# Kernel tuning notes

Measured on AMD Instinct MI355X. Metric: run time of the kernel, lower is better.

Reference implementation:

```python
import jax, jax.numpy as jnp
import numpy as np

N = 50000
E = 800000
IN_C = 128
HID = 64
HEADS = 2
OUT_C = 40
NEG_SLOPE = 0.2


def glorot(key, shape):
    fan_in, fan_out = shape[0], shape[-1]
    lim = jnp.sqrt(6.0 / (fan_in + fan_out))
    return jax.random.uniform(key, shape, jnp.float32, -lim, lim)


def setup_inputs() -> dict:
    key = jax.random.key(0)
    ks = jax.random.split(key, 10)
    x = jax.random.normal(ks[0], (N, IN_C), jnp.float32)
    edge_index = jax.random.randint(ks[1], (2, E), 0, N, jnp.int32)
    # layer 1: heads=2, concat -> out features HEADS*HID
    W1 = glorot(ks[2], (IN_C, HEADS * HID))
    att_src1 = glorot(ks[3], (HEADS, HID))
    att_dst1 = glorot(ks[4], (HEADS, HID))
    b1 = jnp.zeros((HEADS * HID,), jnp.float32)
    # layer 2: out_heads=1, concat=False (mean over the single head)
    W2 = glorot(ks[5], (HEADS * HID, 1 * OUT_C))
    att_src2 = glorot(ks[6], (1, OUT_C))
    att_dst2 = glorot(ks[7], (1, OUT_C))
    b2 = jnp.zeros((OUT_C,), jnp.float32)
    return {"x": x, "edge_index": edge_index,
            "W1": W1, "att_src1": att_src1, "att_dst1": att_dst1, "b1": b1,
            "W2": W2, "att_src2": att_src2, "att_dst2": att_dst2, "b2": b2}


def _segment_softmax(logits, seg, num_segments):
    # logits: [E, H]; softmax over edges sharing the same destination node
    m = jax.ops.segment_max(logits, seg, num_segments=num_segments)
    m = jnp.where(jnp.isfinite(m), m, 0.0)
    e = jnp.exp(logits - m[seg])
    s = jax.ops.segment_sum(e, seg, num_segments=num_segments)
    return e / (s[seg] + 1e-16)


def _gat_conv(x, src, dst, W, a_src, a_dst, b, concat, n_nodes):
    H, C = a_src.shape
    h = (x @ W).reshape(n_nodes, H, C)                    # [N, H, C]
    al_src = jnp.einsum('nhc,hc->nh', h, a_src)           # [N, H]
    al_dst = jnp.einsum('nhc,hc->nh', h, a_dst)           # [N, H]
    e = jax.nn.leaky_relu(al_src[src] + al_dst[dst], NEG_SLOPE)  # [E, H]
    alpha = _segment_softmax(e, dst, n_nodes)             # [E, H]
    msg = h[src] * alpha[:, :, None]                      # [E, H, C]
    out = jax.ops.segment_sum(msg, dst, num_segments=n_nodes)
    out = out.reshape(n_nodes, H * C) if concat else out.mean(axis=1)
    return out + b


def reference(x, edge_index, W1, att_src1, att_dst1, b1, W2, att_src2, att_dst2, b2):
    n_nodes = x.shape[0]
    loop = jnp.arange(n_nodes, dtype=edge_index.dtype)
    src = jnp.concatenate([edge_index[0], loop])  # add self loops
    dst = jnp.concatenate([edge_index[1], loop])
    # eval mode: dropout is identity, use_bn=False -> no batchnorm
    h = _gat_conv(x, src, dst, W1, att_src1, att_dst1, b1, True, n_nodes)
    h = jax.nn.elu(h)
    out = _gat_conv(h, src, dst, W2, att_src2, att_dst2, b2, False, n_nodes)
    return out
```

## Files before the change

kernel.cpp:

```cpp
#include <hip/hip_runtime.h>
#include <hip/hip_fp16.h>

#define NEG_SLOPE 0.2f

typedef _Float16 f16x8 __attribute__((ext_vector_type(8)));
typedef float f32x4 __attribute__((ext_vector_type(4)));

__device__ __forceinline__ int h2i(__half2 h) { return *(int*)&h; }
__device__ __forceinline__ __half2 i2h(int i) { return *(__half2*)&i; }
__device__ __forceinline__ float lrelu(float v) { return (v > 0.f) ? v : NEG_SLOPE * v; }
__device__ __forceinline__ int pkmax(int a, int b) {
    int r;
    asm("v_pk_max_f16 %0, %1, %2" : "=v"(r) : "v"(a), "v"(b));
    return r;
}
__device__ __forceinline__ __half selh(int r, int packed) {
    return (r < 8) ? __low2half(i2h(packed)) : __high2half(i2h(packed));
}

union U16x8 { uint4 u; __half2 h[4]; };
union U16x4 { uint2 u; __half2 h[2]; };

__global__ __launch_bounds__(256) void k_pack(const float* __restrict__ W1,
                                              const float* __restrict__ W2,
                                              _Float16* __restrict__ bp1,
                                              _Float16* __restrict__ bp2,
                                              int* __restrict__ cnt, int N) {
    int idx = blockIdx.x * 256 + threadIdx.x;
    if (idx < N) cnt[idx] = 0;
    if (idx < 16384) {
        int j = idx & 7, l = (idx >> 3) & 63, nt = (idx >> 9) & 7, ks = idx >> 12;
        int k = ks * 32 + (l >> 4) * 8 + j;
        int col = nt * 16 + (l & 15);
        bp1[idx] = (_Float16)W1[k * 128 + col];
    }
    int idx2 = idx - 16384;
    if (idx2 >= 0 && idx2 < 6144) {
        int j = idx2 & 7, l = (idx2 >> 3) & 63, q = idx2 >> 9;
        int nt = q % 3, ks = q / 3;
        int k = ks * 32 + (l >> 4) * 8 + j;
        int col = nt * 16 + (l & 15);
        bp2[idx2] = (col < 40) ? (_Float16)W2[k * 40 + col] : (_Float16)0.f;
    }
}

__global__ void k_bucket(const int* __restrict__ ei, int* __restrict__ cnt,
                         int* __restrict__ colell, int E, int ps) {
    int p = blockIdx.x & 7;
    int e = (blockIdx.x >> 3) * blockDim.x + threadIdx.x;
    if (e >= E) return;
    int d = ei[E + e];
    int lo = p * ps;
    if (d < lo || d >= lo + ps) return;
    int s = ei[e];
    int rank = atomicAdd(&cnt[d], 1);
    if (rank < 64) colell[(size_t)d * 64 + rank] = s;
}

__global__ __launch_bounds__(256) void k_gemm1(
    const float* __restrict__ x, const _Float16* __restrict__ bp1,
    const float* __restrict__ as1, const float* __restrict__ ad1,
    __half2* __restrict__ h1h, float* __restrict__ alsrc, float* __restrict__ aldst,
    int N) {
    int w = threadIdx.x >> 6, l = threadIdx.x & 63;
    int n0 = blockIdx.x * 64 + w * 16;
    int li = l & 15, lg = l >> 4;
    int arow = n0 + li;
    f16x8 a[4];
#pragma unroll
    for (int ks = 0; ks < 4; ks++) {
        float4 p0 = make_float4(0, 0, 0, 0), p1 = make_float4(0, 0, 0, 0);
        if (arow < N) {
            const float4* src = (const float4*)(x + (size_t)arow * 128 + ks * 32 + lg * 8);
            p0 = src[0];
            p1 = src[1];
        }
        f16x8 t;
        t[0] = (_Float16)p0.x; t[1] = (_Float16)p0.y; t[2] = (_Float16)p0.z; t[3] = (_Float16)p0.w;
        t[4] = (_Float16)p1.x; t[5] = (_Float16)p1.y; t[6] = (_Float16)p1.z; t[7] = (_Float16)p1.w;
        a[ks] = t;
    }
    f32x4 acc[8];
#pragma unroll
    for (int nt = 0; nt < 8; nt++) acc[nt] = (f32x4){0.f, 0.f, 0.f, 0.f};
    const f16x8* bp = (const f16x8*)bp1;
#pragma unroll
    for (int nt = 0; nt < 8; nt++)
#pragma unroll
        for (int ks = 0; ks < 4; ks++)
            acc[nt] = __builtin_amdgcn_mfma_f32_16x16x32_f16(a[ks], bp[(ks * 8 + nt) * 64 + l],
                                                             acc[nt], 0, 0, 0);
    float as1v[8], ad1v[8];
#pragma unroll
    for (int nt = 0; nt < 8; nt++) {
        as1v[nt] = as1[nt * 16 + li];
        ad1v[nt] = ad1[nt * 16 + li];
    }
#pragma unroll
    for (int r = 0; r < 4; r++) {
        float ps0 = 0, ps1 = 0, pd0 = 0, pd1 = 0;
#pragma unroll
        for (int nt = 0; nt < 4; nt++) {
            ps0 = fmaf(acc[nt][r], as1v[nt], ps0);
            pd0 = fmaf(acc[nt][r], ad1v[nt], pd0);
        }
#pragma unroll
        for (int nt = 4; nt < 8; nt++) {
            ps1 = fmaf(acc[nt][r], as1v[nt], ps1);
            pd1 = fmaf(acc[nt][r], ad1v[nt], pd1);
        }
#pragma unroll
        for (int o = 1; o < 16; o <<= 1) {
            ps0 += __shfl_xor(ps0, o);
            ps1 += __shfl_xor(ps1, o);
            pd0 += __shfl_xor(pd0, o);
            pd1 += __shfl_xor(pd1, o);
        }
        int node = n0 + lg * 4 + r;
        if (li == 0 && node < N) {
            alsrc[node * 2] = ps0;
            alsrc[node * 2 + 1] = ps1;
            aldst[node * 2] = pd0;
            aldst[node * 2 + 1] = pd1;
        }
    }
#pragma unroll
    for (int nt = 0; nt < 8; nt++)
#pragma unroll
        for (int r = 0; r < 4; r++) {
            float v = acc[nt][r];
            float p = __shfl_down(v, 1);
            int node = n0 + lg * 4 + r;
            if ((l & 1) == 0 && node < N)
                h1h[(size_t)node * 64 + nt * 8 + (li >> 1)] = __floats2half2_rn(v, p);
        }
}

__global__ __launch_bounds__(256) void k_gemm2(
    const _Float16* __restrict__ hf, const _Float16* __restrict__ bp2,
    const float* __restrict__ as2, const float* __restrict__ ad2,
    __half2* __restrict__ h2h, float* __restrict__ alsrc, float* __restrict__ aldst,
    int N) {
    int w = threadIdx.x >> 6, l = threadIdx.x & 63;
    int n0 = blockIdx.x * 64 + w * 16;
    int li = l & 15, lg = l >> 4;
    int arow = n0 + li;
    const f16x8* hfv = (const f16x8*)hf;
    f16x8 a[4];
#pragma unroll
    for (int ks = 0; ks < 4; ks++) {
        f16x8 t;
        if (arow < N) {
            t = hfv[(size_t)arow * 16 + ks * 4 + lg];
        } else {
#pragma unroll
            for (int k = 0; k < 8; k++) t[k] = (_Float16)0.f;
        }
        a[ks] = t;
    }
    f32x4 acc[3];
#pragma unroll
    for (int nt = 0; nt < 3; nt++) acc[nt] = (f32x4){0.f, 0.f, 0.f, 0.f};
    const f16x8* bp = (const f16x8*)bp2;
#pragma unroll
    for (int nt = 0; nt < 3; nt++)
#pragma unroll
        for (int ks = 0; ks < 4; ks++)
            acc[nt] = __builtin_amdgcn_mfma_f32_16x16x32_f16(a[ks], bp[(ks * 3 + nt) * 64 + l],
                                                             acc[nt], 0, 0, 0);
    float as2v[3], ad2v[3];
#pragma unroll
    for (int nt = 0; nt < 3; nt++) {
        int col = nt * 16 + li;
        as2v[nt] = (col < 40) ? as2[col] : 0.f;
        ad2v[nt] = (col < 40) ? ad2[col] : 0.f;
    }
#pragma unroll
    for (int r = 0; r < 4; r++) {
        float ps = 0, pd = 0;
#pragma unroll
        for (int nt = 0; nt < 3; nt++) {
            ps = fmaf(acc[nt][r], as2v[nt], ps);
            pd = fmaf(acc[nt][r], ad2v[nt], pd);
        }
#pragma unroll
        for (int o = 1; o < 16; o <<= 1) {
            ps += __shfl_xor(ps, o);
            pd += __shfl_xor(pd, o);
        }
        int node = n0 + lg * 4 + r;
        if (li == 0 && node < N) {
            alsrc[node] = ps;
            aldst[node] = pd;
        }
    }
#pragma unroll
    for (int nt = 0; nt < 3; nt++)
#pragma unroll
        for (int r = 0; r < 4; r++) {
            float v = acc[nt][r];
            float p = __shfl_down(v, 1);
            int node = n0 + lg * 4 + r;
            int col = nt * 16 + li;
            if ((l & 1) == 0 && col < 40 && node < N)
                h2h[(size_t)node * 20 + nt * 8 + (li >> 1)] = __floats2half2_rn(v, p);
        }
}

__global__ __launch_bounds__(256) void k_gather1(
    const int* __restrict__ cnt, const int* __restrict__ colell,
    const _Float16* __restrict__ h1, const float2* __restrict__ alsrc,
    const float2* __restrict__ aldst, const float4* __restrict__ b1v,
    _Float16* __restrict__ hf, int N) {
    int wid = (int)(((size_t)blockIdx.x * blockDim.x + threadIdx.x) >> 6);
    int lane = threadIdx.x & 63;
    if (wid >= N) return;
    int g = lane >> 4, r = lane & 15;
    float2 asn = alsrc[wid], ad = aldst[wid];
    float ls0 = lrelu(asn.x + ad.x);
    float ls1 = lrelu(asn.y + ad.y);
    int nb = min(cnt[wid], 64);
    int sv = 0;
    float l0 = -1e30f, l1 = -1e30f;
    if (lane < nb) {
        sv = colell[(size_t)wid * 64 + lane];
        float2 av = alsrc[sv];
        l0 = lrelu(av.x + ad.x);
        l1 = lrelu(av.y + ad.y);
    }
    int lpi = h2i(__floats2half2_rn(l0, l1));
#pragma unroll
    for (int o = 32; o > 0; o >>= 1) lpi = pkmax(lpi, __shfl_xor(lpi, o));
    __half2 lp = i2h(lpi);
    float m0 = fmaxf(__low2float(lp), ls0);
    float m1 = fmaxf(__high2float(lp), ls1);
    float e0 = (lane < nb) ? __expf(l0 - m0) : 0.f;
    float e1 = (lane < nb) ? __expf(l1 - m1) : 0.f;
    int we = h2i(__floats2half2_rn(e0, e1));
    float lsh = (r < 8) ? ls0 : ls1;
    float mh = (r < 8) ? m0 : m1;
    __half esh = __float2half((g == 0) ? __expf(lsh - mh) : 0.f);
    float s_part = __half2float(esh);
    __half2 esp = __half2half2(esh);
    U16x8 hs;
    hs.u = *(const uint4*)(h1 + (size_t)wid * 128 + r * 8);
    __half2 a0 = __hmul2(hs.h[0], esp), a1 = __hmul2(hs.h[1], esp),
            a2 = __hmul2(hs.h[2], esp), a3 = __hmul2(hs.h[3], esp);
    if (nb > 0) {
        int i0 = __shfl(sv, g),      p0 = __shfl(we, g);
        int i1 = __shfl(sv, 4 + g),  p1 = __shfl(we, 4 + g);
        int i2 = __shfl(sv, 8 + g),  p2 = __shfl(we, 8 + g);
        int i3 = __shfl(sv, 12 + g), p3 = __shfl(we, 12 + g);
        U16x8 hA, hB, hC, hD;
        hA.u = *(const uint4*)(h1 + (size_t)i0 * 128 + r * 8);
        hB.u = *(const uint4*)(h1 + (size_t)i1 * 128 + r * 8);
        hC.u = *(const uint4*)(h1 + (size_t)i2 * 128 + r * 8);
        hD.u = *(const uint4*)(h1 + (size_t)i3 * 128 + r * 8);
        __half wA = selh(r, p0), wB = selh(r, p1), wC = selh(r, p2), wD = selh(r, p3);
        for (int j = 16; j < nb; j += 4) {
            int i4 = __shfl(sv, j + g), p4 = __shfl(we, j + g);
            U16x8 hN;
            hN.u = *(const uint4*)(h1 + (size_t)i4 * 128 + r * 8);
            __half2 ww = __half2half2(wA);
            s_part += __half2float(wA);
            a0 = __hfma2(ww, hA.h[0], a0);
            a1 = __hfma2(ww, hA.h[1], a1);
            a2 = __hfma2(ww, hA.h[2], a2);
            a3 = __hfma2(ww, hA.h[3], a3);
            hA = hB; wA = wB;
            hB = hC; wB = wC;
            hC = hD; wC = wD;
            hD = hN; wD = selh(r, p4);
        }
        {
            __half2 ww = __half2half2(wA);
            s_part += __half2float(wA);
            a0 = __hfma2(ww, hA.h[0], a0); a1 = __hfma2(ww, hA.h[1], a1);
            a2 = __hfma2(ww, hA.h[2], a2); a3 = __hfma2(ww, hA.h[3], a3);
        }
        {
            __half2 ww = __half2half2(wB);
            s_part += __half2float(wB);
            a0 = __hfma2(ww, hB.h[0], a0); a1 = __hfma2(ww, hB.h[1], a1);
            a2 = __hfma2(ww, hB.h[2], a2); a3 = __hfma2(ww, hB.h[3], a3);
        }
        {
            __half2 ww = __half2half2(wC);
            s_part += __half2float(wC);
            a0 = __hfma2(ww, hC.h[0], a0); a1 = __hfma2(ww, hC.h[1], a1);
            a2 = __hfma2(ww, hC.h[2], a2); a3 = __hfma2(ww, hC.h[3], a3);
        }
        {
            __half2 ww = __half2half2(wD);
            s_part += __half2float(wD);
            a0 = __hfma2(ww, hD.h[0], a0); a1 = __hfma2(ww, hD.h[1], a1);
            a2 = __hfma2(ww, hD.h[2], a2); a3 = __hfma2(ww, hD.h[3], a3);
        }
    }
#pragma unroll
    for (int o = 16; o < 64; o <<= 1) {
        s_part += __shfl_xor(s_part, o);
        a0 = __hadd2(a0, i2h(__shfl_xor(h2i(a0), o)));
        a1 = __hadd2(a1, i2h(__shfl_xor(h2i(a1), o)));
        a2 = __hadd2(a2, i2h(__shfl_xor(h2i(a2), o)));
        a3 = __hadd2(a3, i2h(__shfl_xor(h2i(a3), o)));
    }
    if (g == 0) {
        float inv = 1.f / (s_part + 1e-16f);
        float4 bA = b1v[2 * r], bB = b1v[2 * r + 1];
        float v[8] = {__low2float(a0), __high2float(a0), __low2float(a1), __high2float(a1),
                      __low2float(a2), __high2float(a2), __low2float(a3), __high2float(a3)};
        float vb[8] = {bA.x, bA.y, bA.z, bA.w, bB.x, bB.y, bB.z, bB.w};
        U16x8 o;
#pragma unroll
        for (int k = 0; k < 8; k += 2) {
            float u0 = fmaf(v[k], inv, vb[k]);
            float u1 = fmaf(v[k + 1], inv, vb[k + 1]);
            u0 = (u0 > 0.f) ? u0 : (__expf(u0) - 1.f);
            u1 = (u1 > 0.f) ? u1 : (__expf(u1) - 1.f);
            o.h[k >> 1] = __floats2half2_rn(u0, u1);
        }
        *(uint4*)(hf + (size_t)wid * 128 + r * 8) = o.u;
    }
}

__global__ __launch_bounds__(256) void k_gather2(
    const int* __restrict__ cnt, const int* __restrict__ colell,
    const _Float16* __restrict__ h2, const float* __restrict__ alsrc,
    const float* __restrict__ aldst, const float4* __restrict__ b2v,
    float4* __restrict__ out4, int N) {
    int wid = (int)(((size_t)blockIdx.x * blockDim.x + threadIdx.x) >> 6);
    int lane = threadIdx.x & 63;
    if (wid >= N) return;
    int g = lane >> 4, r = lane & 15;
    int rc = (r < 10) ? r : 0;
    float ad = aldst[wid];
    float ls = lrelu(alsrc[wid] + ad);
    int nb = min(cnt[wid], 64);
    int sv = 0;
    float l = -1e30f;
    if (lane < nb) {
        sv = colell[(size_t)wid * 64 + lane];
        l = lrelu(alsrc[sv] + ad);
    }
    float m = l;
#pragma unroll
    for (int o = 32; o > 0; o >>= 1) m = fmaxf(m, __shfl_xor(m, o));
    m = fmaxf(m, ls);
    float e = (lane < nb) ? __expf(l - m) : 0.f;
    float es = (g == 0) ? __expf(ls - m) : 0.f;
    float s_part = es;
    __half2 esp = __floats2half2_rn(es, es);
    U16x4 hs;
    hs.u = *(const uint2*)(h2 + (size_t)wid * 40 + rc * 4);
    __half2 a0 = __hmul2(hs.h[0], esp), a1 = __hmul2(hs.h[1], esp);
    if (nb > 0) {
        int i0 = __shfl(sv, g);
        int i1 = __shfl(sv, 4 + g);
        int i2 = __shfl(sv, 8 + g);
        int i3 = __shfl(sv, 12 + g);
        float wA = __shfl(e, g), wB = __shfl(e, 4 + g);
        float wC = __shfl(e, 8 + g), wD = __shfl(e, 12 + g);
        U16x4 hA, hB, hC, hD;
        hA.u = *(const uint2*)(h2 + (size_t)i0 * 40 + rc * 4);
        hB.u = *(const uint2*)(h2 + (size_t)i1 * 40 + rc * 4);
        hC.u = *(const uint2*)(h2 + (size_t)i2 * 40 + rc * 4);
        hD.u = *(const uint2*)(h2 + (size_t)i3 * 40 + rc * 4);
        for (int j = 16; j < nb; j += 4) {
            int i4 = __shfl(sv, j + g);
            float wN = __shfl(e, j + g);
            U16x4 hN;
            hN.u = *(const uint2*)(h2 + (size_t)i4 * 40 + rc * 4);
            __half2 ww = __floats2half2_rn(wA, wA);
            s_part += wA;
            a0 = __hfma2(ww, hA.h[0], a0);
            a1 = __hfma2(ww, hA.h[1], a1);
            hA = hB; wA = wB;
            hB = hC; wB = wC;
            hC = hD; wC = wD;
            hD = hN; wD = wN;
        }
        {
            __half2 ww = __floats2half2_rn(wA, wA);
            s_part += wA;
            a0 = __hfma2(ww, hA.h[0], a0); a1 = __hfma2(ww, hA.h[1], a1);
        }
        {
            __half2 ww = __floats2half2_rn(wB, wB);
            s_part += wB;
            a0 = __hfma2(ww, hB.h[0], a0); a1 = __hfma2(ww, hB.h[1], a1);
        }
        {
            __half2 ww = __floats2half2_rn(wC, wC);
            s_part += wC;
            a0 = __hfma2(ww, hC.h[0], a0); a1 = __hfma2(ww, hC.h[1], a1);
        }
        {
            __half2 ww = __floats2half2_rn(wD, wD);
            s_part += wD;
            a0 = __hfma2(ww, hD.h[0], a0); a1 = __hfma2(ww, hD.h[1], a1);
        }
    }
#pragma unroll
    for (int o = 16; o < 64; o <<= 1) {
        s_part += __shfl_xor(s_part, o);
        a0 = __hadd2(a0, i2h(__shfl_xor(h2i(a0), o)));
        a1 = __hadd2(a1, i2h(__shfl_xor(h2i(a1), o)));
    }
    if (g == 0 && r < 10) {
        float inv = 1.f / (s_part + 1e-16f);
        float4 b = b2v[r];
        float4 o = make_float4(fmaf(__low2float(a0), inv, b.x),
                               fmaf(__high2float(a0), inv, b.y),
                               fmaf(__low2float(a1), inv, b.z),
                               fmaf(__high2float(a1), inv, b.w));
        out4[(size_t)wid * 10 + r] = o;
    }
}

extern "C" void kernel_launch(void* const* d_in, const int* in_sizes, int n_in,
                              void* d_out, int out_size, void* d_ws, size_t ws_size,
                              hipStream_t stream) {
    const float* x   = (const float*)d_in[0];
    const int*   ei  = (const int*)d_in[1];
    const float* W1  = (const float*)d_in[2];
    const float* as1 = (const float*)d_in[3];
    const float* ad1 = (const float*)d_in[4];
    const float* b1  = (const float*)d_in[5];
    const float* W2  = (const float*)d_in[6];
    const float* as2 = (const float*)d_in[7];
    const float* ad2 = (const float*)d_in[8];
    const float* b2  = (const float*)d_in[9];
    int N = in_sizes[0] / 128;
    int E = in_sizes[1] / 2;
    float4* out4 = (float4*)d_out;

    char* ws = (char*)d_ws;
    size_t off = 0;
    auto alloc = [&](size_t bytes) {
        char* p = ws + off;
        off += (bytes + 255) & ~(size_t)255;
        return p;
    };
    int*      cnt    = (int*)alloc((size_t)N * 4);
    int*      colell = (int*)alloc((size_t)N * 64 * 4);
    _Float16* bp1    = (_Float16*)alloc(16384 * 2);
    _Float16* bp2    = (_Float16*)alloc(6144 * 2);
    _Float16* h1h    = (_Float16*)alloc((size_t)N * 128 * 2);
    _Float16* hf     = (_Float16*)alloc((size_t)N * 128 * 2);
    _Float16* h2h    = (_Float16*)alloc((size_t)N * 40 * 2);
    float*    alsrc1 = (float*)alloc((size_t)N * 2 * 4);
    float*    aldst1 = (float*)alloc((size_t)N * 2 * 4);
    float*    alsrc2 = (float*)alloc((size_t)N * 4);
    float*    aldst2 = (float*)alloc((size_t)N * 4);

    dim3 b256(256);
    int ps = (N + 7) / 8;
    int gB = 8 * ((E + 255) / 256);
    int gP = (N > 22528 ? N + 255 : 22528 + 255) / 256;

    k_pack<<<gP, b256, 0, stream>>>(W1, W2, bp1, bp2, cnt, N);
    k_bucket<<<gB, b256, 0, stream>>>(ei, cnt, colell, E, ps);

    int gG = (N + 63) / 64;
    k_gemm1<<<gG, b256, 0, stream>>>(x, bp1, as1, ad1, (__half2*)h1h, alsrc1, aldst1, N);
    k_gather1<<<(int)(((size_t)N * 64 + 255) / 256), b256, 0, stream>>>(
        cnt, colell, h1h, (const float2*)alsrc1, (const float2*)aldst1,
        (const float4*)b1, hf, N);

    k_gemm2<<<gG, b256, 0, stream>>>(hf, bp2, as2, ad2, (__half2*)h2h, alsrc2, aldst2, N);
    k_gather2<<<(int)(((size_t)N * 64 + 255) / 256), b256, 0, stream>>>(
        cnt, colell, h2h, alsrc2, aldst2, (const float4*)b2, out4, N);
}
```

Measured before the change: 126.0 us.

## Fuse layer-2 GEMM into layer-1 gather via shared memory; vectorize edge bucketing

The layer-2 projection (MFMA GEMM plus attention logits) now runs inside the layer-1 gather kernel. Each block's four aggregated node rows are staged in LDS and wave 0 does a 16x16 MFMA tile with only 4 valid rows. This drops the hf intermediate buffer and one kernel launch, saving the global write and reread of the hidden features. The cost is a block-wide barrier, three idle waves during the GEMM, and 12 of 16 MFMA rows wasted. Separately, the bucketing kernel now handles two edges per thread using an int2 load of destinations.

```diff
diff --git a/kernel.cpp b/kernel.cpp
--- a/kernel.cpp
+++ b/kernel.cpp
@@ -47,14 +47,20 @@
 __global__ void k_bucket(const int* __restrict__ ei, int* __restrict__ cnt,
                          int* __restrict__ colell, int E, int ps) {
     int p = blockIdx.x & 7;
-    int e = (blockIdx.x >> 3) * blockDim.x + threadIdx.x;
+    int e = ((blockIdx.x >> 3) * blockDim.x + threadIdx.x) * 2;
     if (e >= E) return;
-    int d = ei[E + e];
-    int lo = p * ps;
-    if (d < lo || d >= lo + ps) return;
-    int s = ei[e];
-    int rank = atomicAdd(&cnt[d], 1);
-    if (rank < 64) colell[(size_t)d * 64 + rank] = s;
+    int lo = p * ps, hi = lo + ps;
+    int2 d2 = *(const int2*)(ei + E + e);
+    if (d2.x >= lo && d2.x < hi) {
+        int s = ei[e];
+        int rank = atomicAdd(&cnt[d2.x], 1);
+        if (rank < 64) colell[(size_t)d2.x * 64 + rank] = s;
+    }
+    if (e + 1 < E && d2.y >= lo && d2.y < hi) {
+        int s = ei[e + 1];
+        int rank = atomicAdd(&cnt[d2.y], 1);
+        if (rank < 64) colell[(size_t)d2.y * 64 + rank] = s;
+    }
 }
 
 __global__ __launch_bounds__(256) void k_gemm1(
@@ -136,191 +142,190 @@
         }
 }
 
-__global__ __launch_bounds__(256) void k_gemm2(
-    const _Float16* __restrict__ hf, const _Float16* __restrict__ bp2,
-    const float* __restrict__ as2, const float* __restrict__ ad2,
-    __half2* __restrict__ h2h, float* __restrict__ alsrc, float* __restrict__ aldst,
-    int N) {
-    int w = threadIdx.x >> 6, l = threadIdx.x & 63;
-    int n0 = blockIdx.x * 64 + w * 16;
-    int li = l & 15, lg = l >> 4;
-    int arow = n0 + li;
-    const f16x8* hfv = (const f16x8*)hf;
-    f16x8 a[4];
-#pragma unroll
-    for (int ks = 0; ks < 4; ks++) {
-        f16x8 t;
-        if (arow < N) {
-            t = hfv[(size_t)arow * 16 + ks * 4 + lg];
-        } else {
-#pragma unroll
-            for (int k = 0; k < 8; k++) t[k] = (_Float16)0.f;
-        }
-        a[ks] = t;
-    }
-    f32x4 acc[3];
-#pragma unroll
-    for (int nt = 0; nt < 3; nt++) acc[nt] = (f32x4){0.f, 0.f, 0.f, 0.f};
-    const f16x8* bp = (const f16x8*)bp2;
-#pragma unroll
-    for (int nt = 0; nt < 3; nt++)
-#pragma unroll
-        for (int ks = 0; ks < 4; ks++)
-            acc[nt] = __builtin_amdgcn_mfma_f32_16x16x32_f16(a[ks], bp[(ks * 3 + nt) * 64 + l],
-                                                             acc[nt], 0, 0, 0);
-    float as2v[3], ad2v[3];
-#pragma unroll
-    for (int nt = 0; nt < 3; nt++) {
-        int col = nt * 16 + li;
-        as2v[nt] = (col < 40) ? as2[col] : 0.f;
-        ad2v[nt] = (col < 40) ? ad2[col] : 0.f;
-    }
-#pragma unroll
-    for (int r = 0; r < 4; r++) {
-        float ps = 0, pd = 0;
-#pragma unroll
-        for (int nt = 0; nt < 3; nt++) {
-            ps = fmaf(acc[nt][r], as2v[nt], ps);
-            pd = fmaf(acc[nt][r], ad2v[nt], pd);
-        }
-#pragma unroll
-        for (int o = 1; o < 16; o <<= 1) {
-            ps += __shfl_xor(ps, o);
-            pd += __shfl_xor(pd, o);
-        }
-        int node = n0 + lg * 4 + r;
-        if (li == 0 && node < N) {
-            alsrc[node] = ps;
-            aldst[node] = pd;
-        }
-    }
-#pragma unroll
-    for (int nt = 0; nt < 3; nt++)
-#pragma unroll
-        for (int r = 0; r < 4; r++) {
-            float v = acc[nt][r];
-            float p = __shfl_down(v, 1);
-            int node = n0 + lg * 4 + r;
-            int col = nt * 16 + li;
-            if ((l & 1) == 0 && col < 40 && node < N)
-                h2h[(size_t)node * 20 + nt * 8 + (li >> 1)] = __floats2half2_rn(v, p);
-        }
-}
-
 __global__ __launch_bounds__(256) void k_gather1(
     const int* __restrict__ cnt, const int* __restrict__ colell,
     const _Float16* __restrict__ h1, const float2* __restrict__ alsrc,
     const float2* __restrict__ aldst, const float4* __restrict__ b1v,
-    _Float16* __restrict__ hf, int N) {
-    int wid = (int)(((size_t)blockIdx.x * blockDim.x + threadIdx.x) >> 6);
+    const _Float16* __restrict__ bp2, const float* __restrict__ as2,
+    const float* __restrict__ ad2, __half2* __restrict__ h2h,
+    float* __restrict__ alsrc2, float* __restrict__ aldst2, int N) {
+    __shared__ __align__(16) _Float16 hfl[4][128];
+    int w = threadIdx.x >> 6;
     int lane = threadIdx.x & 63;
-    if (wid >= N) return;
-    int g = lane >> 4, r = lane & 15;
-    float2 asn = alsrc[wid], ad = aldst[wid];
-    float ls0 = lrelu(asn.x + ad.x);
-    float ls1 = lrelu(asn.y + ad.y);
-    int nb = min(cnt[wid], 64);
-    int sv = 0;
-    float l0 = -1e30f, l1 = -1e30f;
-    if (lane < nb) {
-        sv = colell[(size_t)wid * 64 + lane];
-        float2 av = alsrc[sv];
-        l0 = lrelu(av.x + ad.x);
-        l1 = lrelu(av.y + ad.y);
-    }
-    int lpi = h2i(__floats2half2_rn(l0, l1));
-#pragma unroll
-    for (int o = 32; o > 0; o >>= 1) lpi = pkmax(lpi, __shfl_xor(lpi, o));
-    __half2 lp = i2h(lpi);
-    float m0 = fmaxf(__low2float(lp), ls0);
-    float m1 = fmaxf(__high2float(lp), ls1);
-    float e0 = (lane < nb) ? __expf(l0 - m0) : 0.f;
-    float e1 = (lane < nb) ? __expf(l1 - m1) : 0.f;
-    int we = h2i(__floats2half2_rn(e0, e1));
-    float lsh = (r < 8) ? ls0 : ls1;
-    float mh = (r < 8) ? m0 : m1;
-    __half esh = __float2half((g == 0) ? __expf(lsh - mh) : 0.f);
-    float s_part = __half2float(esh);
-    __half2 esp = __half2half2(esh);
-    U16x8 hs;
-    hs.u = *(const uint4*)(h1 + (size_t)wid * 128 + r * 8);
-    __half2 a0 = __hmul2(hs.h[0], esp), a1 = __hmul2(hs.h[1], esp),
-            a2 = __hmul2(hs.h[2], esp), a3 = __hmul2(hs.h[3], esp);
-    if (nb > 0) {
-        int i0 = __shfl(sv, g),      p0 = __shfl(we, g);
-        int i1 = __shfl(sv, 4 + g),  p1 = __shfl(we, 4 + g);
-        int i2 = __shfl(sv, 8 + g),  p2 = __shfl(we, 8 + g);
-        int i3 = __shfl(sv, 12 + g), p3 = __shfl(we, 12 + g);
-        U16x8 hA, hB, hC, hD;
-        hA.u = *(const uint4*)(h1 + (size_t)i0 * 128 + r * 8);
-        hB.u = *(const uint4*)(h1 + (size_t)i1 * 128 + r * 8);
-        hC.u = *(const uint4*)(h1 + (size_t)i2 * 128 + r * 8);
-        hD.u = *(const uint4*)(h1 + (size_t)i3 * 128 + r * 8);
-        __half wA = selh(r, p0), wB = selh(r, p1), wC = selh(r, p2), wD = selh(r, p3);
-        for (int j = 16; j < nb; j += 4) {
-            int i4 = __shfl(sv, j + g), p4 = __shfl(we, j + g);
-            U16x8 hN;
-            hN.u = *(const uint4*)(h1 + (size_t)i4 * 128 + r * 8);
-            __half2 ww = __half2half2(wA);
-            s_part += __half2float(wA);
-            a0 = __hfma2(ww, hA.h[0], a0);
-            a1 = __hfma2(ww, hA.h[1], a1);
-            a2 = __hfma2(ww, hA.h[2], a2);
-            a3 = __hfma2(ww, hA.h[3], a3);
-            hA = hB; wA = wB;
-            hB = hC; wB = wC;
-            hC = hD; wC = wD;
-            hD = hN; wD = selh(r, p4);
-        }
-        {
-            __half2 ww = __half2half2(wA);
-            s_part += __half2float(wA);
-            a0 = __hfma2(ww, hA.h[0], a0); a1 = __hfma2(ww, hA.h[1], a1);
-            a2 = __hfma2(ww, hA.h[2], a2); a3 = __hfma2(ww, hA.h[3], a3);
-        }
-        {
-            __half2 ww = __half2half2(wB);
-            s_part += __half2float(wB);
-            a0 = __hfma2(ww, hB.h[0], a0); a1 = __hfma2(ww, hB.h[1], a1);
-            a2 = __hfma2(ww, hB.h[2], a2); a3 = __hfma2(ww, hB.h[3], a3);
-        }
-        {
-            __half2 ww = __half2half2(wC);
-            s_part += __half2float(wC);
-            a0 = __hfma2(ww, hC.h[0], a0); a1 = __hfma2(ww, hC.h[1], a1);
-            a2 = __hfma2(ww, hC.h[2], a2); a3 = __hfma2(ww, hC.h[3], a3);
-        }
-        {
-            __half2 ww = __half2half2(wD);
-            s_part += __half2float(wD);
-            a0 = __hfma2(ww, hD.h[0], a0); a1 = __hfma2(ww, hD.h[1], a1);
-            a2 = __hfma2(ww, hD.h[2], a2); a3 = __hfma2(ww, hD.h[3], a3);
-        }
-    }
-#pragma unroll
-    for (int o = 16; o < 64; o <<= 1) {
-        s_part += __shfl_xor(s_part, o);
-        a0 = __hadd2(a0, i2h(__shfl_xor(h2i(a0), o)));
-        a1 = __hadd2(a1, i2h(__shfl_xor(h2i(a1), o)));
-        a2 = __hadd2(a2, i2h(__shfl_xor(h2i(a2), o)));
-        a3 = __hadd2(a3, i2h(__shfl_xor(h2i(a3), o)));
-    }
-    if (g == 0) {
-        float inv = 1.f / (s_part + 1e-16f);
-        float4 bA = b1v[2 * r], bB = b1v[2 * r + 1];
-        float v[8] = {__low2float(a0), __high2float(a0), __low2float(a1), __high2float(a1),
-                      __low2float(a2), __high2float(a2), __low2float(a3), __high2float(a3)};
-        float vb[8] = {bA.x, bA.y, bA.z, bA.w, bB.x, bB.y, bB.z, bB.w};
-        U16x8 o;
-#pragma unroll
-        for (int k = 0; k < 8; k += 2) {
-            float u0 = fmaf(v[k], inv, vb[k]);
-            float u1 = fmaf(v[k + 1], inv, vb[k + 1]);
-            u0 = (u0 > 0.f) ? u0 : (__expf(u0) - 1.f);
-            u1 = (u1 > 0.f) ? u1 : (__expf(u1) - 1.f);
-            o.h[k >> 1] = __floats2half2_rn(u0, u1);
-        }
-        *(uint4*)(hf + (size_t)wid * 128 + r * 8) = o.u;
+    int n0 = blockIdx.x * 4;
+    int wid = n0 + w;
+    if (wid < N) {
+        int g = lane >> 4, r = lane & 15;
+        float2 asn = alsrc[wid], ad = aldst[wid];
+        float ls0 = lrelu(asn.x + ad.x);
+        float ls1 = lrelu(asn.y + ad.y);
+        int nb = min(cnt[wid], 64);
+        int sv = 0;
+        float l0 = -1e30f, l1 = -1e30f;
+        if (lane < nb) {
+            sv = colell[(size_t)wid * 64 + lane];
+            float2 av = alsrc[sv];
+            l0 = lrelu(av.x + ad.x);
+            l1 = lrelu(av.y + ad.y);
+        }
+        int lpi = h2i(__floats2half2_rn(l0, l1));
+#pragma unroll
+        for (int o = 32; o > 0; o >>= 1) lpi = pkmax(lpi, __shfl_xor(lpi, o));
+        __half2 lp = i2h(lpi);
+        float m0 = fmaxf(__low2float(lp), ls0);
+        float m1 = fmaxf(__high2float(lp), ls1);
+        float e0 = (lane < nb) ? __expf(l0 - m0) : 0.f;
+        float e1 = (lane < nb) ? __expf(l1 - m1) : 0.f;
+        int we = h2i(__floats2half2_rn(e0, e1));
+        float lsh = (r < 8) ? ls0 : ls1;
+        float mh = (r < 8) ? m0 : m1;
+        __half esh = __float2half((g == 0) ? __expf(lsh - mh) : 0.f);
+        float s_part = __half2float(esh);
+        __half2 esp = __half2half2(esh);
+        U16x8 hs;
+        hs.u = *(const uint4*)(h1 + (size_t)wid * 128 + r * 8);
+        __half2 a0 = __hmul2(hs.h[0], esp), a1 = __hmul2(hs.h[1], esp),
+                a2 = __hmul2(hs.h[2], esp), a3 = __hmul2(hs.h[3], esp);
+        if (nb > 0) {
+            int i0 = __shfl(sv, g),      p0 = __shfl(we, g);
+            int i1 = __shfl(sv, 4 + g),  p1 = __shfl(we, 4 + g);
+            int i2 = __shfl(sv, 8 + g),  p2 = __shfl(we, 8 + g);
+            int i3 = __shfl(sv, 12 + g), p3 = __shfl(we, 12 + g);
+            U16x8 hA, hB, hC, hD;
+            hA.u = *(const uint4*)(h1 + (size_t)i0 * 128 + r * 8);
+            hB.u = *(const uint4*)(h1 + (size_t)i1 * 128 + r * 8);
+            hC.u = *(const uint4*)(h1 + (size_t)i2 * 128 + r * 8);
+            hD.u = *(const uint4*)(h1 + (size_t)i3 * 128 + r * 8);
+            __half wA = selh(r, p0), wB = selh(r, p1), wC = selh(r, p2), wD = selh(r, p3);
+            for (int j = 16; j < nb; j += 4) {
+                int i4 = __shfl(sv, j + g), p4 = __shfl(we, j + g);
+                U16x8 hN;
+                hN.u = *(const uint4*)(h1 + (size_t)i4 * 128 + r * 8);
+                __half2 ww = __half2half2(wA);
+                s_part += __half2float(wA);
+                a0 = __hfma2(ww, hA.h[0], a0);
+                a1 = __hfma2(ww, hA.h[1], a1);
+                a2 = __hfma2(ww, hA.h[2], a2);
+                a3 = __hfma2(ww, hA.h[3], a3);
+                hA = hB; wA = wB;
+                hB = hC; wB = wC;
+                hC = hD; wC = wD;
+                hD = hN; wD = selh(r, p4);
+            }
+            {
+                __half2 ww = __half2half2(wA);
+                s_part += __half2float(wA);
+                a0 = __hfma2(ww, hA.h[0], a0); a1 = __hfma2(ww, hA.h[1], a1);
+                a2 = __hfma2(ww, hA.h[2], a2); a3 = __hfma2(ww, hA.h[3], a3);
+            }
+            {
+                __half2 ww = __half2half2(wB);
+                s_part += __half2float(wB);
+                a0 = __hfma2(ww, hB.h[0], a0); a1 = __hfma2(ww, hB.h[1], a1);
+                a2 = __hfma2(ww, hB.h[2], a2); a3 = __hfma2(ww, hB.h[3], a3);
+            }
+            {
+                __half2 ww = __half2half2(wC);
+                s_part += __half2float(wC);
+                a0 = __hfma2(ww, hC.h[0], a0); a1 = __hfma2(ww, hC.h[1], a1);
+                a2 = __hfma2(ww, hC.h[2], a2); a3 = __hfma2(ww, hC.h[3], a3);
+            }
+            {
+                __half2 ww = __half2half2(wD);
+                s_part += __half2float(wD);
+                a0 = __hfma2(ww, hD.h[0], a0); a1 = __hfma2(ww, hD.h[1], a1);
+                a2 = __hfma2(ww, hD.h[2], a2); a3 = __hfma2(ww, hD.h[3], a3);
+            }
+        }
+#pragma unroll
+        for (int o = 16; o < 64; o <<= 1) {
+            s_part += __shfl_xor(s_part, o);
+            a0 = __hadd2(a0, i2h(__shfl_xor(h2i(a0), o)));
+            a1 = __hadd2(a1, i2h(__shfl_xor(h2i(a1), o)));
+            a2 = __hadd2(a2, i2h(__shfl_xor(h2i(a2), o)));
+            a3 = __hadd2(a3, i2h(__shfl_xor(h2i(a3), o)));
+        }
+        if (g == 0) {
+            float inv = 1.f / (s_part + 1e-16f);
+            float4 bA = b1v[2 * r], bB = b1v[2 * r + 1];
+            float v[8] = {__low2float(a0), __high2float(a0), __low2float(a1), __high2float(a1),
+                          __low2float(a2), __high2float(a2), __low2float(a3), __high2float(a3)};
+            float vb[8] = {bA.x, bA.y, bA.z, bA.w, bB.x, bB.y, bB.z, bB.w};
+            U16x8 o;
+#pragma unroll
+            for (int k = 0; k < 8; k += 2) {
+                float u0 = fmaf(v[k], inv, vb[k]);
+                float u1 = fmaf(v[k + 1], inv, vb[k + 1]);
+                u0 = (u0 > 0.f) ? u0 : (__expf(u0) - 1.f);
+                u1 = (u1 > 0.f) ? u1 : (__expf(u1) - 1.f);
+                o.h[k >> 1] = __floats2half2_rn(u0, u1);
+            }
+            *(uint4*)(&hfl[w][r * 8]) = o.u;
+        }
+    }
+    __syncthreads();
+    if (w == 0) {
+        int li = lane & 15, lg = lane >> 4;
+        f16x8 av[4];
+        const f16x8* hrow = (const f16x8*)(&hfl[li & 3][0]);
+#pragma unroll
+        for (int ks = 0; ks < 4; ks++) {
+            f16x8 t;
+            if (li < 4) {
+                t = hrow[ks * 4 + lg];
+            } else {
+#pragma unroll
+                for (int k = 0; k < 8; k++) t[k] = (_Float16)0.f;
+            }
+            av[ks] = t;
+        }
+        f32x4 acc2[3];
+#pragma unroll
+        for (int nt = 0; nt < 3; nt++) acc2[nt] = (f32x4){0.f, 0.f, 0.f, 0.f};
+        const f16x8* bp = (const f16x8*)bp2;
+#pragma unroll
+        for (int nt = 0; nt < 3; nt++)
+#pragma unroll
+            for (int ks = 0; ks < 4; ks++)
+                acc2[nt] = __builtin_amdgcn_mfma_f32_16x16x32_f16(
+                    av[ks], bp[(ks * 3 + nt) * 64 + lane], acc2[nt], 0, 0, 0);
+        float as2v[3], ad2v[3];
+#pragma unroll
+        for (int nt = 0; nt < 3; nt++) {
+            int col = nt * 16 + li;
+            as2v[nt] = (col < 40) ? as2[col] : 0.f;
+            ad2v[nt] = (col < 40) ? ad2[col] : 0.f;
+        }
+#pragma unroll
+        for (int r = 0; r < 4; r++) {
+            float ps = 0, pd = 0;
+#pragma unroll
+            for (int nt = 0; nt < 3; nt++) {
+                ps = fmaf(acc2[nt][r], as2v[nt], ps);
+                pd = fmaf(acc2[nt][r], ad2v[nt], pd);
+            }
+#pragma unroll
+            for (int o = 1; o < 16; o <<= 1) {
+                ps += __shfl_xor(ps, o);
+                pd += __shfl_xor(pd, o);
+            }
+            int node = n0 + r;
+            if (li == 0 && lg == 0 && node < N) {
+                alsrc2[node] = ps;
+                aldst2[node] = pd;
+            }
+        }
+#pragma unroll
+        for (int nt = 0; nt < 3; nt++)
+#pragma unroll
+            for (int r = 0; r < 4; r++) {
+                float v = acc2[nt][r];
+                float p = __shfl_down(v, 1);
+                int node = n0 + r;
+                int col = nt * 16 + li;
+                if (lg == 0 && (lane & 1) == 0 && col < 40 && node < N)
+                    h2h[(size_t)node * 20 + nt * 8 + (li >> 1)] = __floats2half2_rn(v, p);
+            }
     }
 }
 
@@ -447,7 +452,6 @@
     _Float16* bp1    = (_Float16*)alloc(16384 * 2);
     _Float16* bp2    = (_Float16*)alloc(6144 * 2);
     _Float16* h1h    = (_Float16*)alloc((size_t)N * 128 * 2);
-    _Float16* hf     = (_Float16*)alloc((size_t)N * 128 * 2);
     _Float16* h2h    = (_Float16*)alloc((size_t)N * 40 * 2);
     float*    alsrc1 = (float*)alloc((size_t)N * 2 * 4);
     float*    aldst1 = (float*)alloc((size_t)N * 2 * 4);
@@ -456,7 +460,7 @@
 
     dim3 b256(256);
     int ps = (N + 7) / 8;
-    int gB = 8 * ((E + 255) / 256);
+    int gB = 8 * ((E + 511) / 512);
     int gP = (N > 22528 ? N + 255 : 22528 + 255) / 256;
 
     k_pack<<<gP, b256, 0, stream>>>(W1, W2, bp1, bp2, cnt, N);
@@ -464,11 +468,9 @@
 
     int gG = (N + 63) / 64;
     k_gemm1<<<gG, b256, 0, stream>>>(x, bp1, as1, ad1, (__half2*)h1h, alsrc1, aldst1, N);
-    k_gather1<<<(int)(((size_t)N * 64 + 255) / 256), b256, 0, stream>>>(
+    k_gather1<<<(N + 3) / 4, b256, 0, stream>>>(
         cnt, colell, h1h, (const float2*)alsrc1, (const float2*)aldst1,
-        (const float4*)b1, hf, N);
-
-    k_gemm2<<<gG, b256, 0, stream>>>(hf, bp2, as2, ad2, (__half2*)h2h, alsrc2, aldst2, N);
+        (const float4*)b1, bp2, as2, ad2, (__half2*)h2h, alsrc2, aldst2, N);
     k_gather2<<<(int)(((size_t)N * 64 + 255) / 256), b256, 0, stream>>>(
         cnt, colell, h2h, alsrc2, aldst2, (const float4*)b2, out4, N);
 }
```

Result: no change. 124.7 us (-1.0%).

## Process two destination nodes per wavefront in gathers; vectorize edge bucketing

Applied to the files above, without the earlier changes.

Both gather kernels now map one destination node to each half-wavefront (32 lanes) rather than a full 64-lane wave. Neighbor lists longer than 32 are handled with a second register set, and the loop trip count follows the larger degree of the two halves. With average degree about 16, this cuts the idle lanes and halves the number of waves launched. The bucket kernel reads two destination indices at a time with an int2 load. The cost is divergence between the two nodes sharing a wave and more branching for high-degree nodes.

```diff
diff --git a/kernel.cpp b/kernel.cpp
--- a/kernel.cpp
+++ b/kernel.cpp
@@ -47,14 +47,20 @@
 __global__ void k_bucket(const int* __restrict__ ei, int* __restrict__ cnt,
                          int* __restrict__ colell, int E, int ps) {
     int p = blockIdx.x & 7;
-    int e = (blockIdx.x >> 3) * blockDim.x + threadIdx.x;
+    int e = ((blockIdx.x >> 3) * blockDim.x + threadIdx.x) * 2;
     if (e >= E) return;
-    int d = ei[E + e];
-    int lo = p * ps;
-    if (d < lo || d >= lo + ps) return;
-    int s = ei[e];
-    int rank = atomicAdd(&cnt[d], 1);
-    if (rank < 64) colell[(size_t)d * 64 + rank] = s;
+    int lo = p * ps, hi = lo + ps;
+    int2 d2 = *(const int2*)(ei + E + e);
+    if (d2.x >= lo && d2.x < hi) {
+        int s = ei[e];
+        int rank = atomicAdd(&cnt[d2.x], 1);
+        if (rank < 64) colell[(size_t)d2.x * 64 + rank] = s;
+    }
+    if (e + 1 < E && d2.y >= lo && d2.y < hi) {
+        int s = ei[e + 1];
+        int rank = atomicAdd(&cnt[d2.y], 1);
+        if (rank < 64) colell[(size_t)d2.y * 64 + rank] = s;
+    }
 }
 
 __global__ __launch_bounds__(256) void k_gemm1(
@@ -212,100 +218,122 @@
     const _Float16* __restrict__ h1, const float2* __restrict__ alsrc,
     const float2* __restrict__ aldst, const float4* __restrict__ b1v,
     _Float16* __restrict__ hf, int N) {
-    int wid = (int)(((size_t)blockIdx.x * blockDim.x + threadIdx.x) >> 6);
+    int wave = (int)(((size_t)blockIdx.x * blockDim.x + threadIdx.x) >> 6);
     int lane = threadIdx.x & 63;
-    if (wid >= N) return;
-    int g = lane >> 4, r = lane & 15;
-    float2 asn = alsrc[wid], ad = aldst[wid];
-    float ls0 = lrelu(asn.x + ad.x);
-    float ls1 = lrelu(asn.y + ad.y);
-    int nb = min(cnt[wid], 64);
-    int sv = 0;
-    float l0 = -1e30f, l1 = -1e30f;
-    if (lane < nb) {
-        sv = colell[(size_t)wid * 64 + lane];
-        float2 av = alsrc[sv];
-        l0 = lrelu(av.x + ad.x);
-        l1 = lrelu(av.y + ad.y);
-    }
-    int lpi = h2i(__floats2half2_rn(l0, l1));
-#pragma unroll
-    for (int o = 32; o > 0; o >>= 1) lpi = pkmax(lpi, __shfl_xor(lpi, o));
+    int h = lane >> 5, hl = lane & 31, h32 = h << 5;
+    int wid = wave * 2 + h;
+    bool valid = wid < N;
+    int widc = valid ? wid : 0;
+    int g = hl >> 4, r = hl & 15;
+    float2 asn = alsrc[widc], ad = aldst[widc];
+    float ls0 = valid ? lrelu(asn.x + ad.x) : 0.f;
+    float ls1 = valid ? lrelu(asn.y + ad.y) : 0.f;
+    int nb = valid ? min(cnt[wid], 64) : 0;
+    int nbmax = max(nb, __shfl_xor(nb, 32));
+    bool big = nbmax > 32;
+    int sva = 0;
+    float l0a = -1e30f, l1a = -1e30f;
+    if (hl < nb) {
+        sva = colell[(size_t)wid * 64 + hl];
+        float2 av = alsrc[sva];
+        l0a = lrelu(av.x + ad.x);
+        l1a = lrelu(av.y + ad.y);
+    }
+    int svb = 0, web = 0;
+    float l0b = -1e30f, l1b = -1e30f;
+    if (big && hl + 32 < nb) {
+        svb = colell[(size_t)wid * 64 + 32 + hl];
+        float2 av = alsrc[svb];
+        l0b = lrelu(av.x + ad.x);
+        l1b = lrelu(av.y + ad.y);
+    }
+    int lpi = h2i(__floats2half2_rn(l0a, l1a));
+    if (big) lpi = pkmax(lpi, h2i(__floats2half2_rn(l0b, l1b)));
+#pragma unroll
+    for (int o = 16; o > 0; o >>= 1) lpi = pkmax(lpi, __shfl_xor(lpi, o));
     __half2 lp = i2h(lpi);
     float m0 = fmaxf(__low2float(lp), ls0);
     float m1 = fmaxf(__high2float(lp), ls1);
-    float e0 = (lane < nb) ? __expf(l0 - m0) : 0.f;
-    float e1 = (lane < nb) ? __expf(l1 - m1) : 0.f;
-    int we = h2i(__floats2half2_rn(e0, e1));
+    float e0a = (hl < nb) ? __expf(l0a - m0) : 0.f;
+    float e1a = (hl < nb) ? __expf(l1a - m1) : 0.f;
+    int wea = h2i(__floats2half2_rn(e0a, e1a));
+    if (big) {
+        float e0b = (hl + 32 < nb) ? __expf(l0b - m0) : 0.f;
+        float e1b = (hl + 32 < nb) ? __expf(l1b - m1) : 0.f;
+        web = h2i(__floats2half2_rn(e0b, e1b));
+    }
     float lsh = (r < 8) ? ls0 : ls1;
     float mh = (r < 8) ? m0 : m1;
     __half esh = __float2half((g == 0) ? __expf(lsh - mh) : 0.f);
     float s_part = __half2float(esh);
     __half2 esp = __half2half2(esh);
     U16x8 hs;
-    hs.u = *(const uint4*)(h1 + (size_t)wid * 128 + r * 8);
+    hs.u = *(const uint4*)(h1 + (size_t)widc * 128 + r * 8);
     __half2 a0 = __hmul2(hs.h[0], esp), a1 = __hmul2(hs.h[1], esp),
             a2 = __hmul2(hs.h[2], esp), a3 = __hmul2(hs.h[3], esp);
-    if (nb > 0) {
-        int i0 = __shfl(sv, g),      p0 = __shfl(we, g);
-        int i1 = __shfl(sv, 4 + g),  p1 = __shfl(we, 4 + g);
-        int i2 = __shfl(sv, 8 + g),  p2 = __shfl(we, 8 + g);
-        int i3 = __shfl(sv, 12 + g), p3 = __shfl(we, 12 + g);
-        U16x8 hA, hB, hC, hD;
-        hA.u = *(const uint4*)(h1 + (size_t)i0 * 128 + r * 8);
-        hB.u = *(const uint4*)(h1 + (size_t)i1 * 128 + r * 8);
-        hC.u = *(const uint4*)(h1 + (size_t)i2 * 128 + r * 8);
-        hD.u = *(const uint4*)(h1 + (size_t)i3 * 128 + r * 8);
-        __half wA = selh(r, p0), wB = selh(r, p1), wC = selh(r, p2), wD = selh(r, p3);
-        for (int j = 16; j < nb; j += 4) {
-            int i4 = __shfl(sv, j + g), p4 = __shfl(we, j + g);
-            U16x8 hN;
-            hN.u = *(const uint4*)(h1 + (size_t)i4 * 128 + r * 8);
-            __half2 ww = __half2half2(wA);
-            s_part += __half2float(wA);
-            a0 = __hfma2(ww, hA.h[0], a0);
-            a1 = __hfma2(ww, hA.h[1], a1);
-            a2 = __hfma2(ww, hA.h[2], a2);
-            a3 = __hfma2(ww, hA.h[3], a3);
-            hA = hB; wA = wB;
-            hB = hC; wB = wC;
-            hC = hD; wC = wD;
-            hD = hN; wD = selh(r, p4);
-        }
-        {
-            __half2 ww = __half2half2(wA);
-            s_part += __half2float(wA);
-            a0 = __hfma2(ww, hA.h[0], a0); a1 = __hfma2(ww, hA.h[1], a1);
-            a2 = __hfma2(ww, hA.h[2], a2); a3 = __hfma2(ww, hA.h[3], a3);
-        }
-        {
-            __half2 ww = __half2half2(wB);
-            s_part += __half2float(wB);
-            a0 = __hfma2(ww, hB.h[0], a0); a1 = __hfma2(ww, hB.h[1], a1);
-            a2 = __hfma2(ww, hB.h[2], a2); a3 = __hfma2(ww, hB.h[3], a3);
-        }
-        {
-            __half2 ww = __half2half2(wC);
-            s_part += __half2float(wC);
-            a0 = __hfma2(ww, hC.h[0], a0); a1 = __hfma2(ww, hC.h[1], a1);
-            a2 = __hfma2(ww, hC.h[2], a2); a3 = __hfma2(ww, hC.h[3], a3);
-        }
-        {
-            __half2 ww = __half2half2(wD);
-            s_part += __half2float(wD);
-            a0 = __hfma2(ww, hD.h[0], a0); a1 = __hfma2(ww, hD.h[1], a1);
-            a2 = __hfma2(ww, hD.h[2], a2); a3 = __hfma2(ww, hD.h[3], a3);
-        }
-    }
-#pragma unroll
-    for (int o = 16; o < 64; o <<= 1) {
-        s_part += __shfl_xor(s_part, o);
-        a0 = __hadd2(a0, i2h(__shfl_xor(h2i(a0), o)));
-        a1 = __hadd2(a1, i2h(__shfl_xor(h2i(a1), o)));
-        a2 = __hadd2(a2, i2h(__shfl_xor(h2i(a2), o)));
-        a3 = __hadd2(a3, i2h(__shfl_xor(h2i(a3), o)));
-    }
-    if (g == 0) {
+    int i0 = __shfl(sva, h32 + g),     p0 = __shfl(wea, h32 + g);
+    int i1 = __shfl(sva, h32 + 2 + g), p1 = __shfl(wea, h32 + 2 + g);
+    int i2 = __shfl(sva, h32 + 4 + g), p2 = __shfl(wea, h32 + 4 + g);
+    int i3 = __shfl(sva, h32 + 6 + g), p3 = __shfl(wea, h32 + 6 + g);
+    U16x8 hA, hB, hC, hD;
+    hA.u = *(const uint4*)(h1 + (size_t)i0 * 128 + r * 8);
+    hB.u = *(const uint4*)(h1 + (size_t)i1 * 128 + r * 8);
+    hC.u = *(const uint4*)(h1 + (size_t)i2 * 128 + r * 8);
+    hD.u = *(const uint4*)(h1 + (size_t)i3 * 128 + r * 8);
+    __half wA = selh(r, p0), wB = selh(r, p1), wC = selh(r, p2), wD = selh(r, p3);
+    for (int j = 8; j < nbmax; j += 2) {
+        int slot = j + g;
+        int i4, p4;
+        if (j < 32) {
+            i4 = __shfl(sva, h32 + slot);
+            p4 = __shfl(wea, h32 + slot);
+        } else {
+            i4 = __shfl(svb, h32 + slot - 32);
+            p4 = __shfl(web, h32 + slot - 32);
+        }
+        U16x8 hN;
+        hN.u = *(const uint4*)(h1 + (size_t)i4 * 128 + r * 8);
+        __half2 ww = __half2half2(wA);
+        s_part += __half2float(wA);
+        a0 = __hfma2(ww, hA.h[0], a0);
+        a1 = __hfma2(ww, hA.h[1], a1);
+        a2 = __hfma2(ww, hA.h[2], a2);
+        a3 = __hfma2(ww, hA.h[3], a3);
+        hA = hB; wA = wB;
+        hB = hC; wB = wC;
+        hC = hD; wC = wD;
+        hD = hN; wD = selh(r, p4);
+    }
+    {
+        __half2 ww = __half2half2(wA);
+        s_part += __half2float(wA);
+        a0 = __hfma2(ww, hA.h[0], a0); a1 = __hfma2(ww, hA.h[1], a1);
+        a2 = __hfma2(ww, hA.h[2], a2); a3 = __hfma2(ww, hA.h[3], a3);
+    }
+    {
+        __half2 ww = __half2half2(wB);
+        s_part += __half2float(wB);
+        a0 = __hfma2(ww, hB.h[0], a0); a1 = __hfma2(ww, hB.h[1], a1);
+        a2 = __hfma2(ww, hB.h[2], a2); a3 = __hfma2(ww, hB.h[3], a3);
+    }
+    {
+        __half2 ww = __half2half2(wC);
+        s_part += __half2float(wC);
+        a0 = __hfma2(ww, hC.h[0], a0); a1 = __hfma2(ww, hC.h[1], a1);
+        a2 = __hfma2(ww, hC.h[2], a2); a3 = __hfma2(ww, hC.h[3], a3);
+    }
+    {
+        __half2 ww = __half2half2(wD);
+        s_part += __half2float(wD);
+        a0 = __hfma2(ww, hD.h[0], a0); a1 = __hfma2(ww, hD.h[1], a1);
+        a2 = __hfma2(ww, hD.h[2], a2); a3 = __hfma2(ww, hD.h[3], a3);
+    }
+    s_part += __shfl_xor(s_part, 16);
+    a0 = __hadd2(a0, i2h(__shfl_xor(h2i(a0), 16)));
+    a1 = __hadd2(a1, i2h(__shfl_xor(h2i(a1), 16)));
+    a2 = __hadd2(a2, i2h(__shfl_xor(h2i(a2), 16)));
+    a3 = __hadd2(a3, i2h(__shfl_xor(h2i(a3), 16)));
+    if (g == 0 && valid) {
         float inv = 1.f / (s_part + 1e-16f);
         float4 bA = b1v[2 * r], bB = b1v[2 * r + 1];
         float v[8] = {__low2float(a0), __high2float(a0), __low2float(a1), __high2float(a1),
@@ -329,85 +357,100 @@
     const _Float16* __restrict__ h2, const float* __restrict__ alsrc,
     const float* __restrict__ aldst, const float4* __restrict__ b2v,
     float4* __restrict__ out4, int N) {
-    int wid = (int)(((size_t)blockIdx.x * blockDim.x + threadIdx.x) >> 6);
+    int wave = (int)(((size_t)blockIdx.x * blockDim.x + threadIdx.x) >> 6);
     int lane = threadIdx.x & 63;
-    if (wid >= N) return;
-    int g = lane >> 4, r = lane & 15;
+    int h = lane >> 5, hl = lane & 31, h32 = h << 5;
+    int wid = wave * 2 + h;
+    bool valid = wid < N;
+    int widc = valid ? wid : 0;
+    int g = hl >> 4, r = hl & 15;
     int rc = (r < 10) ? r : 0;
-    float ad = aldst[wid];
-    float ls = lrelu(alsrc[wid] + ad);
-    int nb = min(cnt[wid], 64);
-    int sv = 0;
-    float l = -1e30f;
-    if (lane < nb) {
-        sv = colell[(size_t)wid * 64 + lane];
-        l = lrelu(alsrc[sv] + ad);
-    }
-    float m = l;
-#pragma unroll
-    for (int o = 32; o > 0; o >>= 1) m = fmaxf(m, __shfl_xor(m, o));
+    float ad = valid ? aldst[wid] : 0.f;
+    float ls = valid ? lrelu(alsrc[wid] + ad) : 0.f;
+    int nb = valid ? min(cnt[wid], 64) : 0;
+    int nbmax = max(nb, __shfl_xor(nb, 32));
+    bool big = nbmax > 32;
+    int sva = 0;
+    float la = -1e30f;
+    if (hl < nb) {
+        sva = colell[(size_t)wid * 64 + hl];
+        la = lrelu(alsrc[sva] + ad);
+    }
+    int svb = 0;
+    float lb = -1e30f, eb = 0.f;
+    if (big && hl + 32 < nb) {
+        svb = colell[(size_t)wid * 64 + 32 + hl];
+        lb = lrelu(alsrc[svb] + ad);
+    }
+    float m = fmaxf(la, lb);
+#pragma unroll
+    for (int o = 16; o > 0; o >>= 1) m = fmaxf(m, __shfl_xor(m, o));
     m = fmaxf(m, ls);
-    float e = (lane < nb) ? __expf(l - m) : 0.f;
+    float ea = (hl < nb) ? __expf(la - m) : 0.f;
+    if (big) eb = (hl + 32 < nb) ? __expf(lb - m) : 0.f;
     float es = (g == 0) ? __expf(ls - m) : 0.f;
     float s_part = es;
     __half2 esp = __floats2half2_rn(es, es);
     U16x4 hs;
-    hs.u = *(const uint2*)(h2 + (size_t)wid * 40 + rc * 4);
+    hs.u = *(const uint2*)(h2 + (size_t)widc * 40 + rc * 4);
     __half2 a0 = __hmul2(hs.h[0], esp), a1 = __hmul2(hs.h[1], esp);
-    if (nb > 0) {
-        int i0 = __shfl(sv, g);
-        int i1 = __shfl(sv, 4 + g);
-        int i2 = __shfl(sv, 8 + g);
-        int i3 = __shfl(sv, 12 + g);
-        float wA = __shfl(e, g), wB = __shfl(e, 4 + g);
-        float wC = __shfl(e, 8 + g), wD = __shfl(e, 12 + g);
-        U16x4 hA, hB, hC, hD;
-        hA.u = *(const uint2*)(h2 + (size_t)i0 * 40 + rc * 4);
-        hB.u = *(const uint2*)(h2 + (size_t)i1 * 40 + rc * 4);
-        hC.u = *(const uint2*)(h2 + (size_t)i2 * 40 + rc * 4);
-        hD.u = *(const uint2*)(h2 + (size_t)i3 * 40 + rc * 4);
-        for (int j = 16; j < nb; j += 4) {
-            int i4 = __shfl(sv, j + g);
-            float wN = __shfl(e, j + g);
-            U16x4 hN;
-            hN.u = *(const uint2*)(h2 + (size_t)i4 * 40 + rc * 4);
-            __half2 ww = __floats2half2_rn(wA, wA);
-            s_part += wA;
-            a0 = __hfma2(ww, hA.h[0], a0);
-            a1 = __hfma2(ww, hA.h[1], a1);
-            hA = hB; wA = wB;
-            hB = hC; wB = wC;
-            hC = hD; wC = wD;
-            hD = hN; wD = wN;
-        }
-        {
-            __half2 ww = __floats2half2_rn(wA, wA);
-            s_part += wA;
-            a0 = __hfma2(ww, hA.h[0], a0); a1 = __hfma2(ww, hA.h[1], a1);
-        }
-        {
-            __half2 ww = __floats2half2_rn(wB, wB);
-            s_part += wB;
-            a0 = __hfma2(ww, hB.h[0], a0); a1 = __hfma2(ww, hB.h[1], a1);
-        }
-        {
-            __half2 ww = __floats2half2_rn(wC, wC);
-            s_part += wC;
-            a0 = __hfma2(ww, hC.h[0], a0); a1 = __hfma2(ww, hC.h[1], a1);
-        }
-        {
-            __half2 ww = __floats2half2_rn(wD, wD);
-            s_part += wD;
-            a0 = __hfma2(ww, hD.h[0], a0); a1 = __hfma2(ww, hD.h[1], a1);
-        }
-    }
-#pragma unroll
-    for (int o = 16; o < 64; o <<= 1) {
-        s_part += __shfl_xor(s_part, o);
-        a0 = __hadd2(a0, i2h(__shfl_xor(h2i(a0), o)));
-        a1 = __hadd2(a1, i2h(__shfl_xor(h2i(a1), o)));
-    }
-    if (g == 0 && r < 10) {
+    int i0 = __shfl(sva, h32 + g);
+    int i1 = __shfl(sva, h32 + 2 + g);
+    int i2 = __shfl(sva, h32 + 4 + g);
+    int i3 = __shfl(sva, h32 + 6 + g);
+    float wA = __shfl(ea, h32 + g), wB = __shfl(ea, h32 + 2 + g);
+    float wC = __shfl(ea, h32 + 4 + g), wD = __shfl(ea, h32 + 6 + g);
+    U16x4 hA, hB, hC, hD;
+    hA.u = *(const uint2*)(h2 + (size_t)i0 * 40 + rc * 4);
+    hB.u = *(const uint2*)(h2 + (size_t)i1 * 40 + rc * 4);
+    hC.u = *(const uint2*)(h2 + (size_t)i2 * 40 + rc * 4);
+    hD.u = *(const uint2*)(h2 + (size_t)i3 * 40 + rc * 4);
+    for (int j = 8; j < nbmax; j += 2) {
+        int slot = j + g;
+        int i4;
+        float wN;
+        if (j < 32) {
+            i4 = __shfl(sva, h32 + slot);
+            wN = __shfl(ea, h32 + slot);
+        } else {
+            i4 = __shfl(svb, h32 + slot - 32);
+            wN = __shfl(eb, h32 + slot - 32);
+        }
+        U16x4 hN;
+        hN.u = *(const uint2*)(h2 + (size_t)i4 * 40 + rc * 4);
+        __half2 ww = __floats2half2_rn(wA, wA);
+        s_part += wA;
+        a0 = __hfma2(ww, hA.h[0], a0);
+        a1 = __hfma2(ww, hA.h[1], a1);
+        hA = hB; wA = wB;
+        hB = hC; wB = wC;
+        hC = hD; wC = wD;
+        hD = hN; wD = wN;
+    }
+    {
+        __half2 ww = __floats2half2_rn(wA, wA);
+        s_part += wA;
+        a0 = __hfma2(ww, hA.h[0], a0); a1 = __hfma2(ww, hA.h[1], a1);
+    }
+    {
+        __half2 ww = __floats2half2_rn(wB, wB);
+        s_part += wB;
+        a0 = __hfma2(ww, hB.h[0], a0); a1 = __hfma2(ww, hB.h[1], a1);
+    }
+    {
+        __half2 ww = __floats2half2_rn(wC, wC);
+        s_part += wC;
+        a0 = __hfma2(ww, hC.h[0], a0); a1 = __hfma2(ww, hC.h[1], a1);
+    }
+    {
+        __half2 ww = __floats2half2_rn(wD, wD);
+        s_part += wD;
+        a0 = __hfma2(ww, hD.h[0], a0); a1 = __hfma2(ww, hD.h[1], a1);
+    }
+    s_part += __shfl_xor(s_part, 16);
+    a0 = __hadd2(a0, i2h(__shfl_xor(h2i(a0), 16)));
+    a1 = __hadd2(a1, i2h(__shfl_xor(h2i(a1), 16)));
+    if (g == 0 && r < 10 && valid) {
         float inv = 1.f / (s_part + 1e-16f);
         float4 b = b2v[r];
         float4 o = make_float4(fmaf(__low2float(a0), inv, b.x),
@@ -456,19 +499,21 @@
 
     dim3 b256(256);
     int ps = (N + 7) / 8;
-    int gB = 8 * ((E + 255) / 256);
+    int gB = 8 * ((E + 511) / 512);
     int gP = (N > 22528 ? N + 255 : 22528 + 255) / 256;
 
     k_pack<<<gP, b256, 0, stream>>>(W1, W2, bp1, bp2, cnt, N);
     k_bucket<<<gB, b256, 0, stream>>>(ei, cnt, colell, E, ps);
 
     int gG = (N + 63) / 64;
+    int nwaves = (N + 1) / 2;
+    int gGa = (nwaves + 3) / 4;
+
     k_gemm1<<<gG, b256, 0, stream>>>(x, bp1, as1, ad1, (__half2*)h1h, alsrc1, aldst1, N);
-    k_gather1<<<(int)(((size_t)N * 64 + 255) / 256), b256, 0, stream>>>(
+    k_gather1<<<gGa, b256, 0, stream>>>(
         cnt, colell, h1h, (const float2*)alsrc1, (const float2*)aldst1,
         (const float4*)b1, hf, N);
-
     k_gemm2<<<gG, b256, 0, stream>>>(hf, bp2, as2, ad2, (__half2*)h2h, alsrc2, aldst2, N);
-    k_gather2<<<(int)(((size_t)N * 64 + 255) / 256), b256, 0, stream>>>(
+    k_gather2<<<gGa, b256, 0, stream>>>(
         cnt, colell, h2h, alsrc2, aldst2, (const float4*)b2, out4, N);
 }
```

After: 125.9 us. No clear change (-0.0%).
